# Kernel tuning notes

Hardware: AMD Instinct MI355X
Metric: run time of the kernel (lower is better)

## Reference

```python
import jax, jax.numpy as jnp
import numpy as np

N = 128          # system size (8*8*2), hard-coded in SpectrumLoss
M_LANCZOS = 10   # Lanczos(m=10)
KAPPA = 0.276


def dd_opt(x, U1, kappa):
    # Wilson-style 2D hopping operator (stand-in for the external DDOpt).
    # x: (B,8,8,2) fields, U1: (B,8,8,2) real gauge links (2 directions).
    u0 = U1[..., 0:1]
    u1 = U1[..., 1:2]
    hop = (u0 * jnp.roll(x, -1, axis=1)
           + u1 * jnp.roll(x, -1, axis=2)
           + jnp.roll(u0 * x, 1, axis=1)
           + jnp.roll(u1 * x, 1, axis=2))
    return x - kappa * hop


def build_lower_tri(net_out):
    # Row-major packing of a lower-triangular NxN matrix (torch.tril_indices order).
    B = net_out.shape[0]
    r, c = jnp.tril_indices(N)
    L = jnp.zeros((B, N, N), net_out.dtype)
    return L.at[:, r, c].set(net_out)


def matvect(L, U1, x):
    # x: (B, N). Preconditioned operator: L (L^T (D x)).
    B = x.shape[0]
    y = dd_opt(x.reshape(B, 8, 8, 2), U1, KAPPA).reshape(B, N)
    y = jnp.einsum('bij,bi->bj', L, y)  # upper_tri_mat: M^H v (real -> M^T v)
    y = jnp.einsum('bij,bj->bi', L, y)  # lower_tri_matvect: L v
    return y


def lanczos(Av, v0):
    # Standard batched Lanczos producing symmetric tridiagonal T (B, M, M).
    B = v0.shape[0]

    def step(carry, _):
        v_prev, v_cur, beta = carry
        w = Av(v_cur)
        alpha = jnp.sum(w * v_cur, axis=1)
        w = w - alpha[:, None] * v_cur - beta[:, None] * v_prev
        beta_new = jnp.linalg.norm(w, axis=1)
        v_next = w / (beta_new[:, None] + 1e-30)
        return (v_cur, v_next, beta_new), (alpha, beta_new)

    init = (jnp.zeros_like(v0), v0, jnp.zeros((B,), v0.dtype))
    _, (alphas, betas) = jax.lax.scan(step, init, None, length=M_LANCZOS)
    alphas = alphas.T  # (B, M)
    betas = betas.T    # (B, M); last beta unused
    T = jnp.zeros((B, M_LANCZOS, M_LANCZOS), v0.dtype)
    i = jnp.arange(M_LANCZOS)
    T = T.at[:, i, i].set(alphas)
    j = jnp.arange(M_LANCZOS - 1)
    T = T.at[:, j, j + 1].set(betas[:, :-1])
    T = T.at[:, j + 1, j].set(betas[:, :-1])
    return T


def setup_inputs() -> dict:
    key = jax.random.key(0)
    k1, k2, k3 = jax.random.split(key, 3)
    B = 2048
    net_out = jax.random.normal(k1, (B, N * (N + 1) // 2), dtype=jnp.float32)
    U1 = jax.random.uniform(k2, (B, 8, 8, 2), dtype=jnp.float32)
    v = jax.random.normal(k3, (B, N), dtype=jnp.float32)
    return {"net_out": net_out, "U1": U1, "v": v}


def reference(net_out, U1, v):
    vn = v / jnp.linalg.norm(v, axis=1, keepdims=True)
    L = build_lower_tri(net_out)
    T = lanczos(lambda x: matvect(L, U1, x), vn)
    eig = jnp.abs(jnp.linalg.eigvalsh(T))  # symmetric tridiagonal -> real eigvals
    max_e = jnp.max(eig, axis=1)
    min_e = jnp.min(eig, axis=1)
    return jnp.mean(max_e ** 2) - jnp.mean(min_e ** 2)
```

## Files before the change

kernel.cpp:

```cpp
#include <hip/hip_runtime.h>
#include <hip/hip_bf16.h>
#include <math.h>

#define NN 128
#define TRI 8256
#define BATCH 2048
#define M_L 10
#define KAPPA 0.276f
#define LDL 136

using half8  = __attribute__((ext_vector_type(8))) _Float16;
using half2v = __attribute__((ext_vector_type(2))) _Float16;
using f32x4  = __attribute__((ext_vector_type(4))) float;

static __device__ inline float dot2h(unsigned m, unsigned y, float c) {
#if __has_builtin(__builtin_amdgcn_fdot2)
    return __builtin_amdgcn_fdot2(__builtin_bit_cast(half2v, m),
                                  __builtin_bit_cast(half2v, y), c, false);
#else
    half2v a = __builtin_bit_cast(half2v, m), b = __builtin_bit_cast(half2v, y);
    return c + (float)a.x * (float)b.x + (float)a.y * (float)b.y;
#endif
}

__global__ __launch_bounds__(256, 2) void lanczos_kernel(
    const float* __restrict__ net_out,
    const float* __restrict__ U1,
    const float* __restrict__ v_in,
    float* __restrict__ ab_out)
{
    __shared__ __align__(16) _Float16 Lsq[128 * LDL];
    __shared__ __align__(16) unsigned yscr[4][64];

    const int t = threadIdx.x;
    const int lane = t & 63;
    const int w = t >> 6;
    const int myb = blockIdx.x * 4 + w;

    unsigned m0[64], m1[64];
    float x0 = 0.f, x1 = 0.f, p0 = 0.f, p1 = 0.f, beta = 0.f;
    float u0c = 0.f, u1c = 0.f, u0m = 0.f, u1m = 0.f;

    for (int q = 0; q < 4; q++) {
        const int b = blockIdx.x * 4 + q;

        {
            unsigned long long* z = (unsigned long long*)Lsq;
            #pragma unroll
            for (int k = t; k < 128 * LDL / 4; k += 256) z[k] = 0ULL;
        }
        __syncthreads();

        {
            const float4* src4 = (const float4*)(net_out + (size_t)b * TRI);
            for (int qd = t; qd < TRI / 4; qd += 256) {
                float4 f = src4[qd];
                int e = 4 * qd;
                int r = (int)((sqrtf(8.0f * (float)e + 1.0f) - 1.0f) * 0.5f);
                while ((r + 1) * (r + 2) / 2 <= e) r++;
                while (r * (r + 1) / 2 > e) r--;
                int c = e - r * (r + 1) / 2;
                Lsq[r * LDL + c] = (_Float16)f.x;
                c++; if (c > r) { r++; c = 0; }
                Lsq[r * LDL + c] = (_Float16)f.y;
                c++; if (c > r) { r++; c = 0; }
                Lsq[r * LDL + c] = (_Float16)f.z;
                c++; if (c > r) { r++; c = 0; }
                Lsq[r * LDL + c] = (_Float16)f.w;
            }
        }
        __syncthreads();

        {
            const int m = lane & 15;
            const int g = lane >> 4;
            f32x4 acc[2][8];
            #pragma unroll
            for (int bi = 0; bi < 2; bi++)
                #pragma unroll
                for (int j = 0; j < 8; j++) acc[bi][j] = (f32x4){0.f, 0.f, 0.f, 0.f};
            const int band0 = w, band1 = w + 4;
            #pragma unroll
            for (int kc = 0; kc < 4; kc++) {
                const int col = kc * 32 + g * 8;
                half8 a0 = *(const half8*)&Lsq[(16 * band0 + m) * LDL + col];
                half8 a1 = *(const half8*)&Lsq[(16 * band1 + m) * LDL + col];
                #pragma unroll
                for (int j = 0; j < 8; j++) {
                    half8 bfr = *(const half8*)&Lsq[(16 * j + m) * LDL + col];
                    acc[0][j] = __builtin_amdgcn_mfma_f32_16x16x32_f16(a0, bfr, acc[0][j], 0, 0, 0);
                    acc[1][j] = __builtin_amdgcn_mfma_f32_16x16x32_f16(a1, bfr, acc[1][j], 0, 0, 0);
                }
            }
            __syncthreads();

            #pragma unroll
            for (int bi = 0; bi < 2; bi++) {
                const int band = (bi == 0) ? band0 : band1;
                #pragma unroll
                for (int j = 0; j < 8; j++) {
                    f32x4 a = acc[bi][j];
                    half2v p01 = {(_Float16)a[0], (_Float16)a[1]};
                    half2v p23 = {(_Float16)a[2], (_Float16)a[3]};
                    uint2 pk;
                    pk.x = __builtin_bit_cast(unsigned, p01);
                    pk.y = __builtin_bit_cast(unsigned, p23);
                    *(uint2*)&Lsq[(16 * j + m) * LDL + 16 * band + 4 * g] = pk;
                }
            }
        }
        __syncthreads();

        if (w == q) {
            #pragma unroll
            for (int c = 0; c < 16; c++) {
                uint4 a = *(const uint4*)&Lsq[(2 * lane) * LDL + 8 * c];
                m0[4 * c] = a.x; m0[4 * c + 1] = a.y; m0[4 * c + 2] = a.z; m0[4 * c + 3] = a.w;
                uint4 bb = *(const uint4*)&Lsq[(2 * lane + 1) * LDL + 8 * c];
                m1[4 * c] = bb.x; m1[4 * c + 1] = bb.y; m1[4 * c + 2] = bb.z; m1[4 * c + 3] = bb.w;
            }
            float2 vv = *(const float2*)(v_in + (size_t)b * NN + 2 * lane);
            float s = vv.x * vv.x + vv.y * vv.y;
            #pragma unroll
            for (int o = 1; o < 64; o <<= 1) s += __shfl_xor(s, o, 64);
            float inv = 1.0f / sqrtf(s);
            x0 = vv.x * inv; x1 = vv.y * inv;
            float2 uu = *(const float2*)(U1 + (size_t)b * 128 + 2 * lane);
            u0c = uu.x; u1c = uu.y;
            u0m = __shfl(u0c, (lane + 56) & 63, 64);
            u1m = __shfl(u1c, (lane & 56) | ((lane + 7) & 7), 64);
        }
        __syncthreads();
    }

    unsigned* ys = yscr[w];
    const int l_ip = (lane + 8) & 63;
    const int l_jp = (lane & 56) | ((lane + 1) & 7);
    const int l_im = (lane + 56) & 63;
    const int l_jm = (lane & 56) | ((lane + 7) & 7);

    for (int it = 0; it < M_L; it++) {
        float a0 = __shfl(x0, l_ip, 64), a1 = __shfl(x1, l_ip, 64);
        float b0 = __shfl(x0, l_jp, 64), b1 = __shfl(x1, l_jp, 64);
        float c0 = __shfl(x0, l_im, 64), c1 = __shfl(x1, l_im, 64);
        float d0 = __shfl(x0, l_jm, 64), d1 = __shfl(x1, l_jm, 64);
        float y0 = x0 - KAPPA * (u0c * a0 + u1c * b0 + u0m * c0 + u1m * d0);
        float y1 = x1 - KAPPA * (u0c * a1 + u1c * b1 + u0m * c1 + u1m * d1);

        half2v yp = {(_Float16)y0, (_Float16)y1};
        ys[lane] = __builtin_bit_cast(unsigned, yp);

        float z0 = 0.f, z1 = 0.f;
        #pragma unroll
        for (int c = 0; c < 16; c++) {
            uint4 yv = *(const uint4*)&ys[4 * c];
            z0 = dot2h(m0[4 * c],     yv.x, z0);
            z1 = dot2h(m1[4 * c],     yv.x, z1);
            z0 = dot2h(m0[4 * c + 1], yv.y, z0);
            z1 = dot2h(m1[4 * c + 1], yv.y, z1);
            z0 = dot2h(m0[4 * c + 2], yv.z, z0);
            z1 = dot2h(m1[4 * c + 2], yv.z, z1);
            z0 = dot2h(m0[4 * c + 3], yv.w, z0);
            z1 = dot2h(m1[4 * c + 3], yv.w, z1);
        }

        float s1 = z0 * x0 + z1 * x1;
        float s2 = z0 * z0 + z1 * z1;
        float s3 = z0 * p0 + z1 * p1;
        #pragma unroll
        for (int o = 1; o < 64; o <<= 1) {
            s1 += __shfl_xor(s1, o, 64);
            s2 += __shfl_xor(s2, o, 64);
            s3 += __shfl_xor(s3, o, 64);
        }

        float alpha = s1;
        float b2 = s2 - alpha * alpha - beta * (2.0f * s3 - beta);
        float bn = sqrtf(fmaxf(b2, 0.0f));
        float w0 = z0 - alpha * x0 - beta * p0;
        float w1 = z1 - alpha * x1 - beta * p1;
        float inv = 1.0f / (bn + 1e-30f);
        p0 = x0; p1 = x1;
        x0 = w0 * inv; x1 = w1 * inv;
        beta = bn;
        if (lane == 0) {
            ab_out[(size_t)myb * 20 + it]      = alpha;
            ab_out[(size_t)myb * 20 + 10 + it] = bn;
        }
    }
}

__device__ inline int sturm_count10(const double* a, const double* off2, double x) {
    double pm = 1.0;
    double p  = a[0] - x;
    int c = (p < 0.0);
    #pragma unroll
    for (int i = 1; i < M_L; i++) {
        double pn = (a[i] - x) * p - off2[i - 1] * pm;
        c += ((pn < 0.0) != (p < 0.0));
        if (fabs(pn) > 1e150) { pn *= 1e-150; p *= 1e-150; }
        pm = p; p = pn;
    }
    return c;
}

__device__ inline double msect_smallest(const double* a, const double* off2,
                                        double lo, double hi, int K, int lane) {
    for (int round = 0; round < 4; round++) {
        double wdt = (hi - lo) * (1.0 / 65.0);
        double x = lo + wdt * (double)(lane + 1);
        int cnt = sturm_count10(a, off2, x);
        unsigned long long mask = __ballot(cnt >= K);
        if (mask == 0ULL) {
            lo = lo + wdt * 64.0;
        } else {
            int p = __ffsll(mask) - 1;
            hi = lo + wdt * (double)(p + 1);
            if (p > 0) lo = lo + wdt * (double)p;
        }
    }
    return 0.5 * (lo + hi);
}

__device__ inline double msect_window(const double* a, const double* off2,
                                      double maxabs, int lane) {
    double lo = 0.0, hi = maxabs;
    for (int round = 0; round < 4; round++) {
        double wdt = (hi - lo) * (1.0 / 65.0);
        double s = lo + wdt * (double)(lane + 1);
        int inwin = sturm_count10(a, off2, s) - sturm_count10(a, off2, -s);
        unsigned long long mask = __ballot(inwin >= 1);
        if (mask == 0ULL) {
            lo = lo + wdt * 64.0;
        } else {
            int p = __ffsll(mask) - 1;
            hi = lo + wdt * (double)(p + 1);
            if (p > 0) lo = lo + wdt * (double)p;
        }
    }
    return 0.5 * (lo + hi);
}

__global__ __launch_bounds__(256) void eig_kernel(
    const float* __restrict__ ab, float* __restrict__ contrib)
{
    const int lane = threadIdx.x & 63;
    const int b = blockIdx.x * 4 + (threadIdx.x >> 6);
    if (b >= BATCH) return;
    const float* p = ab + (size_t)b * 20;
    double a[M_L], off2[M_L - 1], offa[M_L - 1];
    #pragma unroll
    for (int i = 0; i < M_L; i++) a[i] = (double)p[i];
    #pragma unroll
    for (int i = 0; i < M_L - 1; i++) {
        double bb = (double)p[10 + i];
        offa[i] = fabs(bb);
        off2[i] = bb * bb;
    }
    double lo = 1e300, hi = -1e300;
    #pragma unroll
    for (int i = 0; i < M_L; i++) {
        double r = 0.0;
        if (i > 0) r += offa[i - 1];
        if (i < M_L - 1) r += offa[i];
        lo = fmin(lo, a[i] - r);
        hi = fmax(hi, a[i] + r);
    }
    double lmax = msect_smallest(a, off2, lo, hi, M_L, lane);
    double lmin = msect_smallest(a, off2, lo, hi, 1,   lane);
    double maxabs = fmax(fabs(lmax), fabs(lmin));
    double minabs = msect_window(a, off2, maxabs, lane);
    if (lane == 0) contrib[b] = (float)(maxabs * maxabs - minabs * minabs);
}

__global__ __launch_bounds__(1024) void reduce_kernel(
    const float* __restrict__ contrib, float* __restrict__ out)
{
    __shared__ float red[16];
    int t = threadIdx.x;
    float s = contrib[t] + contrib[t + 1024];
    #pragma unroll
    for (int o = 32; o > 0; o >>= 1) s += __shfl_down(s, o, 64);
    if ((t & 63) == 0) red[t >> 6] = s;
    __syncthreads();
    if (t < 64) {
        float r = (t < 16) ? red[t] : 0.0f;
        #pragma unroll
        for (int o = 8; o > 0; o >>= 1) r += __shfl_down(r, o, 64);
        if (t == 0) out[0] = r / (float)BATCH;
    }
}

extern "C" void kernel_launch(void* const* d_in, const int* in_sizes, int n_in,
                              void* d_out, int out_size, void* d_ws, size_t ws_size,
                              hipStream_t stream) {
    const float* net_out = (const float*)d_in[0];
    const float* U1      = (const float*)d_in[1];
    const float* v       = (const float*)d_in[2];
    float* ab      = (float*)d_ws;
    float* contrib = ab + (size_t)BATCH * 20;

    lanczos_kernel<<<BATCH / 4, 256, 0, stream>>>(net_out, U1, v, ab);
    eig_kernel<<<BATCH / 4, 256, 0, stream>>>(ab, contrib);
    reduce_kernel<<<1, 1024, 0, stream>>>(contrib, (float*)d_out);
}
```

Before: 143.7 us.

## Assign one batch element per block and split Lanczos matvec across all warps

Each block now handles a single batch element instead of four processed serially. The Lanczos matvec is split across all 256 threads, each computing half a row from shared memory, with partials reduced by warp 0. Previously one warp per element held the matrix in 128 registers per lane. Launch bounds rise to 4 blocks per CU, trading register-resident matrix data for LDS reads and two block barriers per iteration in exchange for better occupancy and more parallelism.

```diff
diff --git a/kernel.cpp b/kernel.cpp
--- a/kernel.cpp
+++ b/kernel.cpp
@@ -23,170 +23,183 @@
 #endif
 }
 
-__global__ __launch_bounds__(256, 2) void lanczos_kernel(
+__global__ __launch_bounds__(256, 4) void lanczos_kernel(
     const float* __restrict__ net_out,
     const float* __restrict__ U1,
     const float* __restrict__ v_in,
     float* __restrict__ ab_out)
 {
     __shared__ __align__(16) _Float16 Lsq[128 * LDL];
-    __shared__ __align__(16) unsigned yscr[4][64];
-
+    __shared__ __align__(16) unsigned ys[64];
+    __shared__ __align__(16) float part[256];
+
+    const int b = blockIdx.x;
     const int t = threadIdx.x;
     const int lane = t & 63;
     const int w = t >> 6;
-    const int myb = blockIdx.x * 4 + w;
-
-    unsigned m0[64], m1[64];
+
+    {
+        unsigned long long* z = (unsigned long long*)Lsq;
+        #pragma unroll
+        for (int k = t; k < 128 * LDL / 4; k += 256) z[k] = 0ULL;
+    }
+    __syncthreads();
+
+    {
+        const float4* src4 = (const float4*)(net_out + (size_t)b * TRI);
+        for (int q = t; q < TRI / 4; q += 256) {
+            float4 f = src4[q];
+            int e = 4 * q;
+            int r = (int)((sqrtf(8.0f * (float)e + 1.0f) - 1.0f) * 0.5f);
+            while ((r + 1) * (r + 2) / 2 <= e) r++;
+            while (r * (r + 1) / 2 > e) r--;
+            int c = e - r * (r + 1) / 2;
+            Lsq[r * LDL + c] = (_Float16)f.x;
+            c++; if (c > r) { r++; c = 0; }
+            Lsq[r * LDL + c] = (_Float16)f.y;
+            c++; if (c > r) { r++; c = 0; }
+            Lsq[r * LDL + c] = (_Float16)f.z;
+            c++; if (c > r) { r++; c = 0; }
+            Lsq[r * LDL + c] = (_Float16)f.w;
+        }
+    }
+    __syncthreads();
+
+    {
+        const int m = lane & 15;
+        const int g = lane >> 4;
+        f32x4 acc[2][8];
+        #pragma unroll
+        for (int bi = 0; bi < 2; bi++)
+            #pragma unroll
+            for (int j = 0; j < 8; j++) acc[bi][j] = (f32x4){0.f, 0.f, 0.f, 0.f};
+        const int band0 = w, band1 = w + 4;
+        #pragma unroll
+        for (int kc = 0; kc < 4; kc++) {
+            const int col = kc * 32 + g * 8;
+            half8 a0 = *(const half8*)&Lsq[(16 * band0 + m) * LDL + col];
+            half8 a1 = *(const half8*)&Lsq[(16 * band1 + m) * LDL + col];
+            #pragma unroll
+            for (int j = 0; j < 8; j++) {
+                half8 bfr = *(const half8*)&Lsq[(16 * j + m) * LDL + col];
+                acc[0][j] = __builtin_amdgcn_mfma_f32_16x16x32_f16(a0, bfr, acc[0][j], 0, 0, 0);
+                acc[1][j] = __builtin_amdgcn_mfma_f32_16x16x32_f16(a1, bfr, acc[1][j], 0, 0, 0);
+            }
+        }
+        __syncthreads();
+
+        #pragma unroll
+        for (int bi = 0; bi < 2; bi++) {
+            const int band = (bi == 0) ? band0 : band1;
+            #pragma unroll
+            for (int j = 0; j < 8; j++) {
+                f32x4 a = acc[bi][j];
+                half2v p01 = {(_Float16)a[0], (_Float16)a[1]};
+                half2v p23 = {(_Float16)a[2], (_Float16)a[3]};
+                uint2 pk;
+                pk.x = __builtin_bit_cast(unsigned, p01);
+                pk.y = __builtin_bit_cast(unsigned, p23);
+                *(uint2*)&Lsq[(16 * j + m) * LDL + 16 * band + 4 * g] = pk;
+            }
+        }
+    }
+    __syncthreads();
+
     float x0 = 0.f, x1 = 0.f, p0 = 0.f, p1 = 0.f, beta = 0.f;
     float u0c = 0.f, u1c = 0.f, u0m = 0.f, u1m = 0.f;
-
-    for (int q = 0; q < 4; q++) {
-        const int b = blockIdx.x * 4 + q;
-
-        {
-            unsigned long long* z = (unsigned long long*)Lsq;
-            #pragma unroll
-            for (int k = t; k < 128 * LDL / 4; k += 256) z[k] = 0ULL;
-        }
-        __syncthreads();
-
-        {
-            const float4* src4 = (const float4*)(net_out + (size_t)b * TRI);
-            for (int qd = t; qd < TRI / 4; qd += 256) {
-                float4 f = src4[qd];
-                int e = 4 * qd;
-                int r = (int)((sqrtf(8.0f * (float)e + 1.0f) - 1.0f) * 0.5f);
-                while ((r + 1) * (r + 2) / 2 <= e) r++;
-                while (r * (r + 1) / 2 > e) r--;
-                int c = e - r * (r + 1) / 2;
-                Lsq[r * LDL + c] = (_Float16)f.x;
-                c++; if (c > r) { r++; c = 0; }
-                Lsq[r * LDL + c] = (_Float16)f.y;
-                c++; if (c > r) { r++; c = 0; }
-                Lsq[r * LDL + c] = (_Float16)f.z;
-                c++; if (c > r) { r++; c = 0; }
-                Lsq[r * LDL + c] = (_Float16)f.w;
-            }
-        }
-        __syncthreads();
-
-        {
-            const int m = lane & 15;
-            const int g = lane >> 4;
-            f32x4 acc[2][8];
-            #pragma unroll
-            for (int bi = 0; bi < 2; bi++)
-                #pragma unroll
-                for (int j = 0; j < 8; j++) acc[bi][j] = (f32x4){0.f, 0.f, 0.f, 0.f};
-            const int band0 = w, band1 = w + 4;
-            #pragma unroll
-            for (int kc = 0; kc < 4; kc++) {
-                const int col = kc * 32 + g * 8;
-                half8 a0 = *(const half8*)&Lsq[(16 * band0 + m) * LDL + col];
-                half8 a1 = *(const half8*)&Lsq[(16 * band1 + m) * LDL + col];
-                #pragma unroll
-                for (int j = 0; j < 8; j++) {
-                    half8 bfr = *(const half8*)&Lsq[(16 * j + m) * LDL + col];
-                    acc[0][j] = __builtin_amdgcn_mfma_f32_16x16x32_f16(a0, bfr, acc[0][j], 0, 0, 0);
-                    acc[1][j] = __builtin_amdgcn_mfma_f32_16x16x32_f16(a1, bfr, acc[1][j], 0, 0, 0);
-                }
-            }
-            __syncthreads();
-
-            #pragma unroll
-            for (int bi = 0; bi < 2; bi++) {
-                const int band = (bi == 0) ? band0 : band1;
-                #pragma unroll
-                for (int j = 0; j < 8; j++) {
-                    f32x4 a = acc[bi][j];
-                    half2v p01 = {(_Float16)a[0], (_Float16)a[1]};
-                    half2v p23 = {(_Float16)a[2], (_Float16)a[3]};
-                    uint2 pk;
-                    pk.x = __builtin_bit_cast(unsigned, p01);
-                    pk.y = __builtin_bit_cast(unsigned, p23);
-                    *(uint2*)&Lsq[(16 * j + m) * LDL + 16 * band + 4 * g] = pk;
-                }
-            }
-        }
-        __syncthreads();
-
-        if (w == q) {
-            #pragma unroll
-            for (int c = 0; c < 16; c++) {
-                uint4 a = *(const uint4*)&Lsq[(2 * lane) * LDL + 8 * c];
-                m0[4 * c] = a.x; m0[4 * c + 1] = a.y; m0[4 * c + 2] = a.z; m0[4 * c + 3] = a.w;
-                uint4 bb = *(const uint4*)&Lsq[(2 * lane + 1) * LDL + 8 * c];
-                m1[4 * c] = bb.x; m1[4 * c + 1] = bb.y; m1[4 * c + 2] = bb.z; m1[4 * c + 3] = bb.w;
-            }
-            float2 vv = *(const float2*)(v_in + (size_t)b * NN + 2 * lane);
-            float s = vv.x * vv.x + vv.y * vv.y;
-            #pragma unroll
-            for (int o = 1; o < 64; o <<= 1) s += __shfl_xor(s, o, 64);
-            float inv = 1.0f / sqrtf(s);
-            x0 = vv.x * inv; x1 = vv.y * inv;
-            float2 uu = *(const float2*)(U1 + (size_t)b * 128 + 2 * lane);
-            u0c = uu.x; u1c = uu.y;
-            u0m = __shfl(u0c, (lane + 56) & 63, 64);
-            u1m = __shfl(u1c, (lane & 56) | ((lane + 7) & 7), 64);
-        }
-        __syncthreads();
-    }
-
-    unsigned* ys = yscr[w];
     const int l_ip = (lane + 8) & 63;
     const int l_jp = (lane & 56) | ((lane + 1) & 7);
     const int l_im = (lane + 56) & 63;
     const int l_jm = (lane & 56) | ((lane + 7) & 7);
 
-    for (int it = 0; it < M_L; it++) {
+    if (w == 0) {
+        float2 vv = *(const float2*)(v_in + (size_t)b * NN + 2 * lane);
+        float s = vv.x * vv.x + vv.y * vv.y;
+        #pragma unroll
+        for (int o = 1; o < 64; o <<= 1) s += __shfl_xor(s, o, 64);
+        float inv = 1.0f / sqrtf(s);
+        x0 = vv.x * inv; x1 = vv.y * inv;
+        float2 uu = *(const float2*)(U1 + (size_t)b * 128 + 2 * lane);
+        u0c = uu.x; u1c = uu.y;
+        u0m = __shfl(u0c, l_im, 64);
+        u1m = __shfl(u1c, l_jm, 64);
+
         float a0 = __shfl(x0, l_ip, 64), a1 = __shfl(x1, l_ip, 64);
         float b0 = __shfl(x0, l_jp, 64), b1 = __shfl(x1, l_jp, 64);
         float c0 = __shfl(x0, l_im, 64), c1 = __shfl(x1, l_im, 64);
         float d0 = __shfl(x0, l_jm, 64), d1 = __shfl(x1, l_jm, 64);
         float y0 = x0 - KAPPA * (u0c * a0 + u1c * b0 + u0m * c0 + u1m * d0);
         float y1 = x1 - KAPPA * (u0c * a1 + u1c * b1 + u0m * c1 + u1m * d1);
-
         half2v yp = {(_Float16)y0, (_Float16)y1};
         ys[lane] = __builtin_bit_cast(unsigned, yp);
-
-        float z0 = 0.f, z1 = 0.f;
-        #pragma unroll
-        for (int c = 0; c < 16; c++) {
-            uint4 yv = *(const uint4*)&ys[4 * c];
-            z0 = dot2h(m0[4 * c],     yv.x, z0);
-            z1 = dot2h(m1[4 * c],     yv.x, z1);
-            z0 = dot2h(m0[4 * c + 1], yv.y, z0);
-            z1 = dot2h(m1[4 * c + 1], yv.y, z1);
-            z0 = dot2h(m0[4 * c + 2], yv.z, z0);
-            z1 = dot2h(m1[4 * c + 2], yv.z, z1);
-            z0 = dot2h(m0[4 * c + 3], yv.w, z0);
-            z1 = dot2h(m1[4 * c + 3], yv.w, z1);
-        }
-
-        float s1 = z0 * x0 + z1 * x1;
-        float s2 = z0 * z0 + z1 * z1;
-        float s3 = z0 * p0 + z1 * p1;
-        #pragma unroll
-        for (int o = 1; o < 64; o <<= 1) {
-            s1 += __shfl_xor(s1, o, 64);
-            s2 += __shfl_xor(s2, o, 64);
-            s3 += __shfl_xor(s3, o, 64);
-        }
-
-        float alpha = s1;
-        float b2 = s2 - alpha * alpha - beta * (2.0f * s3 - beta);
-        float bn = sqrtf(fmaxf(b2, 0.0f));
-        float w0 = z0 - alpha * x0 - beta * p0;
-        float w1 = z1 - alpha * x1 - beta * p1;
-        float inv = 1.0f / (bn + 1e-30f);
-        p0 = x0; p1 = x1;
-        x0 = w0 * inv; x1 = w1 * inv;
-        beta = bn;
-        if (lane == 0) {
-            ab_out[(size_t)myb * 20 + it]      = alpha;
-            ab_out[(size_t)myb * 20 + 10 + it] = bn;
-        }
+    }
+    __syncthreads();
+
+    const int r = t & 127, h = t >> 7;
+    const uint4* M4 = (const uint4*)&Lsq[r * LDL + 64 * h];
+    const uint4* Y4 = (const uint4*)&ys[32 * h];
+
+    for (int it = 0; it < M_L; it++) {
+        {
+            float aA = 0.f, aB = 0.f, aC = 0.f, aD = 0.f;
+            #pragma unroll
+            for (int c = 0; c < 8; c += 4) {
+                uint4 m_0 = M4[c],     y_0 = Y4[c];
+                uint4 m_1 = M4[c + 1], y_1 = Y4[c + 1];
+                uint4 m_2 = M4[c + 2], y_2 = Y4[c + 2];
+                uint4 m_3 = M4[c + 3], y_3 = Y4[c + 3];
+                aA = dot2h(m_0.x, y_0.x, aA); aA = dot2h(m_0.y, y_0.y, aA);
+                aA = dot2h(m_0.z, y_0.z, aA); aA = dot2h(m_0.w, y_0.w, aA);
+                aB = dot2h(m_1.x, y_1.x, aB); aB = dot2h(m_1.y, y_1.y, aB);
+                aB = dot2h(m_1.z, y_1.z, aB); aB = dot2h(m_1.w, y_1.w, aB);
+                aC = dot2h(m_2.x, y_2.x, aC); aC = dot2h(m_2.y, y_2.y, aC);
+                aC = dot2h(m_2.z, y_2.z, aC); aC = dot2h(m_2.w, y_2.w, aC);
+                aD = dot2h(m_3.x, y_3.x, aD); aD = dot2h(m_3.y, y_3.y, aD);
+                aD = dot2h(m_3.z, y_3.z, aD); aD = dot2h(m_3.w, y_3.w, aD);
+            }
+            part[t] = (aA + aB) + (aC + aD);
+        }
+        __syncthreads();
+
+        if (w == 0) {
+            float2 pa = *(const float2*)&part[2 * lane];
+            float2 pb = *(const float2*)&part[128 + 2 * lane];
+            float z0 = pa.x + pb.x;
+            float z1 = pa.y + pb.y;
+
+            float s1 = z0 * x0 + z1 * x1;
+            float s2 = z0 * z0 + z1 * z1;
+            float s3 = z0 * p0 + z1 * p1;
+            #pragma unroll
+            for (int o = 1; o < 64; o <<= 1) {
+                s1 += __shfl_xor(s1, o, 64);
+                s2 += __shfl_xor(s2, o, 64);
+                s3 += __shfl_xor(s3, o, 64);
+            }
+            float alpha = s1;
+            float b2 = s2 - alpha * alpha - beta * (2.0f * s3 - beta);
+            float bn = sqrtf(fmaxf(b2, 0.0f));
+            float w0 = z0 - alpha * x0 - beta * p0;
+            float w1 = z1 - alpha * x1 - beta * p1;
+            float inv = 1.0f / (bn + 1e-30f);
+            p0 = x0; p1 = x1;
+            x0 = w0 * inv; x1 = w1 * inv;
+            beta = bn;
+            if (lane == 0) {
+                ab_out[(size_t)b * 20 + it]      = alpha;
+                ab_out[(size_t)b * 20 + 10 + it] = bn;
+            }
+
+            float a0 = __shfl(x0, l_ip, 64), a1 = __shfl(x1, l_ip, 64);
+            float b0 = __shfl(x0, l_jp, 64), b1 = __shfl(x1, l_jp, 64);
+            float c0 = __shfl(x0, l_im, 64), c1 = __shfl(x1, l_im, 64);
+            float d0 = __shfl(x0, l_jm, 64), d1 = __shfl(x1, l_jm, 64);
+            float y0 = x0 - KAPPA * (u0c * a0 + u1c * b0 + u0m * c0 + u1m * d0);
+            float y1 = x1 - KAPPA * (u0c * a1 + u1c * b1 + u0m * c1 + u1m * d1);
+            half2v yp = {(_Float16)y0, (_Float16)y1};
+            ys[lane] = __builtin_bit_cast(unsigned, yp);
+        }
+        __syncthreads();
     }
 }
 
@@ -300,7 +313,7 @@
     float* ab      = (float*)d_ws;
     float* contrib = ab + (size_t)BATCH * 20;
 
-    lanczos_kernel<<<BATCH / 4, 256, 0, stream>>>(net_out, U1, v, ab);
+    lanczos_kernel<<<BATCH, 256, 0, stream>>>(net_out, U1, v, ab);
     eig_kernel<<<BATCH / 4, 256, 0, stream>>>(ab, contrib);
     reduce_kernel<<<1, 1024, 0, stream>>>(contrib, (float*)d_out);
 }
```

After: 137.6 us. -4.3%, faster.
